# Performance work log

Measured on AMD Instinct MI355X. Metric: run time of the kernel, lower is better.

## Reference

```python
import jax, jax.numpy as jnp
import numpy as np

B, N = 16, 256
RMIN, RC_S, NSHIFTS = 0.8, 5.0, 16


def setup_inputs() -> dict:
    key = jax.random.key(0)
    # positions scaled so typical pair distances span [0, rc_s]
    coord = jax.random.normal(key, (B, N, 3), dtype=jnp.float32) * 3.0
    eta = jnp.float32((1.0 / ((RC_S - RMIN) / NSHIFTS)) ** 2)
    shifts = jnp.linspace(RMIN, RC_S, NSHIFTS + 1, dtype=jnp.float32)[:NSHIFTS]
    return {
        "coord": coord,
        "shifts_s": shifts,
        "eta_s": eta,
        "rc_s": jnp.float32(RC_S),
    }


def reference(coord, shifts_s, eta_s, rc_s):
    # coord: [B, N, 3]
    n = coord.shape[1]
    eye = jnp.eye(n, dtype=bool)  # self-pair mask
    # r_ij = r_j - r_i : [B, N, N, 3]
    r_ij = coord[:, None, :, :] - coord[:, :, None, :]
    sq = jnp.sum(r_ij * r_ij, axis=-1)
    # safe sqrt on diagonal, then fill self-distances with rc_s (dmat_fill)
    d = jnp.sqrt(jnp.where(eye, 1.0, sq))
    d_ij = jnp.where(eye, rc_s, d)  # [B, N, N]
    # cosine cutoff, masked to 0 on invalid (self) pairs
    fc = jnp.where(d_ij < rc_s, 0.5 * jnp.cos(jnp.pi * d_ij / rc_s) + 0.5, 0.0)
    fc = jnp.where(eye, 0.0, fc)
    # Gaussian basis expansion * cutoff: gs [B, N, N, nshifts]
    gs = jnp.exp(-eta_s * (d_ij[..., None] - shifts_s) ** 2) * fc[..., None]
    # unit vectors
    u_ij = r_ij / d_ij[..., None]  # [B, N, N, 3]
    # outer product vector features: gv [B, N, N, 3, nshifts]
    gv = gs[..., None, :] * u_ij[..., None]
    return d_ij, gs, gv
```

## Files before the change

### kernel.cpp

```cpp
#include <hip/hip_runtime.h>
#include <math.h>

#define BB   16
#define NN_  256
#define NSH  16

__global__ __launch_bounds__(256) void aev_sv_kernel(
    const float* __restrict__ coord,
    const float* __restrict__ shifts,
    const float* __restrict__ eta_p,
    const float* __restrict__ rc_p,
    float* __restrict__ out)
{
    const int p = blockIdx.x * blockDim.x + threadIdx.x;
    const int NNsq = NN_ * NN_;
    const int b  = p >> 16;
    const int ij = p & (NNsq - 1);
    const int i  = ij >> 8;
    const int j  = ij & (NN_ - 1);

    const float rc  = rc_p[0];
    const float eta = eta_p[0];

    const float* ci = coord + ((size_t)b * NN_ + i) * 3;
    const float* cj = coord + ((size_t)b * NN_ + j) * 3;
    const float dx = cj[0] - ci[0];
    const float dy = cj[1] - ci[1];
    const float dz = cj[2] - ci[2];
    const float sq = dx * dx + dy * dy + dz * dz;

    float d, fc;
    if (i == j) {
        d  = rc;
        fc = 0.0f;
    } else {
        d  = sqrtf(sq);
        fc = (d < rc) ? (0.5f * cospif(d / rc) + 0.5f) : 0.0f;
    }

    const float inv_d = 1.0f / d;
    const float ux = dx * inv_d;
    const float uy = dy * inv_d;
    const float uz = dz * inv_d;

    float gs[NSH];
#pragma unroll
    for (int k = 0; k < NSH; ++k) {
        const float t = d - shifts[k];
        gs[k] = expf(-eta * t * t) * fc;
    }

    const size_t BNN = (size_t)BB * NNsq;

    out[p] = d;

    float4* gs_out = (float4*)(out + BNN + (size_t)p * NSH);
#pragma unroll
    for (int q = 0; q < 4; ++q)
        gs_out[q] = make_float4(gs[4 * q + 0], gs[4 * q + 1],
                                gs[4 * q + 2], gs[4 * q + 3]);

    float* gv_base = out + BNN + BNN * (size_t)NSH + (size_t)p * 3 * NSH;
    const float u[3] = {ux, uy, uz};
#pragma unroll
    for (int c = 0; c < 3; ++c) {
        float4* gv_out = (float4*)(gv_base + c * NSH);
#pragma unroll
        for (int q = 0; q < 4; ++q)
            gv_out[q] = make_float4(gs[4 * q + 0] * u[c], gs[4 * q + 1] * u[c],
                                    gs[4 * q + 2] * u[c], gs[4 * q + 3] * u[c]);
    }
}

extern "C" void kernel_launch(void* const* d_in, const int* in_sizes, int n_in,
                              void* d_out, int out_size, void* d_ws, size_t ws_size,
                              hipStream_t stream) {
    const float* coord  = (const float*)d_in[0];
    const float* shifts = (const float*)d_in[1];
    const float* eta    = (const float*)d_in[2];
    const float* rc     = (const float*)d_in[3];
    float* out = (float*)d_out;

    const int total = BB * NN_ * NN_;
    const int block = 256;
    const int grid  = total / block;
    aev_sv_kernel<<<grid, block, 0, stream>>>(coord, shifts, eta, rc, out);
}
```

Baseline: 299.7 us.

## Split each pair across four threads for coalesced float4 output stores

Each pair is now handled by four threads, and each thread computes four of the sixteen Gaussian shifts. Adjacent lanes therefore write adjacent float4 chunks of gs and gv, which makes the stores coalesced where before each thread wrote a 256-byte strided run. The cost is that distance, cosine cutoff and the unit vector are computed redundantly in all four threads, and four times as many threads are launched. The kernel is store-bound (about 68 MB of output), so better coalescing of writes is the intended gain.

After: 263.7 us. 1.14x faster.

```diff
diff --git a/kernel.cpp b/kernel.cpp
--- a/kernel.cpp
+++ b/kernel.cpp
@@ -12,18 +12,19 @@
     const float* __restrict__ rc_p,
     float* __restrict__ out)
 {
-    const int p = blockIdx.x * blockDim.x + threadIdx.x;
-    const int NNsq = NN_ * NN_;
+    const int tid = blockIdx.x * blockDim.x + threadIdx.x;
+    const int p = tid >> 2;
+    const int q = tid & 3;
     const int b  = p >> 16;
-    const int ij = p & (NNsq - 1);
+    const int ij = p & 65535;
     const int i  = ij >> 8;
-    const int j  = ij & (NN_ - 1);
+    const int j  = ij & 255;
 
     const float rc  = rc_p[0];
     const float eta = eta_p[0];
 
-    const float* ci = coord + ((size_t)b * NN_ + i) * 3;
-    const float* cj = coord + ((size_t)b * NN_ + j) * 3;
+    const float* ci = coord + (b * NN_ + i) * 3;
+    const float* cj = coord + (b * NN_ + j) * 3;
     const float dx = cj[0] - ci[0];
     const float dy = cj[1] - ci[1];
     const float dz = cj[2] - ci[2];
@@ -43,33 +44,27 @@
     const float uy = dy * inv_d;
     const float uz = dz * inv_d;
 
-    float gs[NSH];
-#pragma unroll
-    for (int k = 0; k < NSH; ++k) {
-        const float t = d - shifts[k];
-        gs[k] = expf(-eta * t * t) * fc;
-    }
+    const float4 sh = ((const float4*)shifts)[q];
+    const float neta = -eta;
+    const float t0 = d - sh.x, t1 = d - sh.y, t2 = d - sh.z, t3 = d - sh.w;
+    const float g0 = expf(neta * t0 * t0) * fc;
+    const float g1 = expf(neta * t1 * t1) * fc;
+    const float g2 = expf(neta * t2 * t2) * fc;
+    const float g3 = expf(neta * t3 * t3) * fc;
 
-    const size_t BNN = (size_t)BB * NNsq;
+    constexpr int BNN = BB * NN_ * NN_;
+    constexpr size_t GS_OFF = (size_t)BNN;
+    constexpr size_t GV_OFF = GS_OFF + (size_t)BNN * NSH;
 
-    out[p] = d;
+    if (q == 0) out[p] = d;
 
-    float4* gs_out = (float4*)(out + BNN + (size_t)p * NSH);
-#pragma unroll
-    for (int q = 0; q < 4; ++q)
-        gs_out[q] = make_float4(gs[4 * q + 0], gs[4 * q + 1],
-                                gs[4 * q + 2], gs[4 * q + 3]);
+    float4* gs_out = (float4*)(out + GS_OFF);
+    gs_out[p * 4 + q] = make_float4(g0, g1, g2, g3);
 
-    float* gv_base = out + BNN + BNN * (size_t)NSH + (size_t)p * 3 * NSH;
-    const float u[3] = {ux, uy, uz};
-#pragma unroll
-    for (int c = 0; c < 3; ++c) {
-        float4* gv_out = (float4*)(gv_base + c * NSH);
-#pragma unroll
-        for (int q = 0; q < 4; ++q)
-            gv_out[q] = make_float4(gs[4 * q + 0] * u[c], gs[4 * q + 1] * u[c],
-                                    gs[4 * q + 2] * u[c], gs[4 * q + 3] * u[c]);
-    }
+    float4* gv_out = (float4*)(out + GV_OFF);
+    gv_out[p * 12 + 0 * 4 + q] = make_float4(g0 * ux, g1 * ux, g2 * ux, g3 * ux);
+    gv_out[p * 12 + 1 * 4 + q] = make_float4(g0 * uy, g1 * uy, g2 * uy, g3 * uy);
+    gv_out[p * 12 + 2 * 4 + q] = make_float4(g0 * uz, g1 * uz, g2 * uz, g3 * uz);
 }
 
 extern "C" void kernel_launch(void* const* d_in, const int* in_sizes, int n_in,
@@ -81,7 +76,7 @@
     const float* rc     = (const float*)d_in[3];
     float* out = (float*)d_out;
 
-    const int total = BB * NN_ * NN_;
+    const int total = BB * NN_ * NN_ * 4;
     const int block = 256;
     const int grid  = total / block;
     aev_sv_kernel<<<grid, block, 0, stream>>>(coord, shifts, eta, rc, out);
```
